# Kernel tuning notes

Measured on AMD Instinct MI355X. Metric: run time of the kernel, lower is better.

Reference implementation:

```python
import jax, jax.numpy as jnp
import numpy as np

B, L, D, H = 2, 2048, 1024, 16
DH = D // H  # dim_head = 64
NEG_INF = 1e12


def setup_inputs() -> dict:
    key = jax.random.key(0)
    ks = jax.random.split(key, 12)
    s_in = 1.0 / np.sqrt(D)
    inp = {
        "q": jax.random.normal(ks[0], (B, L, D), jnp.float32),
        "k": jax.random.normal(ks[1], (B, L, D), jnp.float32),
        "v": jax.random.normal(ks[2], (B, L, D), jnp.float32),
        # causal mask, True = position is masked (matches masked_fill_ semantics)
        "mask": jnp.broadcast_to(
            jnp.triu(jnp.ones((L, L), jnp.bool_), k=1)[None, None], (B, 1, L, L)
        ),
        # torch Linear weight is [out, in]; store transposed [in, out] for x @ W
        "Wq": jax.random.normal(ks[3], (D, D), jnp.float32) * s_in,
        "bq": jnp.zeros((D,), jnp.float32),
        "Wk": jax.random.normal(ks[4], (D, D), jnp.float32) * s_in,
        "bk": jnp.zeros((D,), jnp.float32),
        "Wv": jax.random.normal(ks[5], (D, D), jnp.float32) * s_in,
        "bv": jnp.zeros((D,), jnp.float32),
        "Wo": jax.random.normal(ks[6], (D, D), jnp.float32) * s_in,
        "bo": jnp.zeros((D,), jnp.float32),
    }
    return inp


def _split_heads(x):
    # [b, l, h*d] -> [b, h, l, d]
    b, l, _ = x.shape
    return x.reshape(b, l, H, DH).transpose(0, 2, 1, 3)


def reference(q, k, v, mask, Wq, bq, Wk, bk, Wv, bv, Wo, bo):
    Q = _split_heads(q @ Wq + bq)
    K = _split_heads(k @ Wk + bk)
    V = _split_heads(v @ Wv + bv)
    scale = 1.0 / np.sqrt(DH)
    dots = jnp.einsum("bhqd,bhkd->bhqk", Q, K) * scale  # [b, h, L, L]
    dots = jnp.where(mask, -NEG_INF, dots)
    attn = jax.nn.softmax(dots, axis=-1)
    out = jnp.einsum("bhqk,bhkd->bhqd", attn, V)  # [b, h, L, d]
    out = out.transpose(0, 2, 1, 3).reshape(q.shape[0], q.shape[1], D)
    return out @ Wo + bo
```

## Files before the change

### kernel.cpp

```cpp
#include <hip/hip_runtime.h>
#include <stdint.h>

typedef __bf16 bf16;
typedef bf16 bf16x8 __attribute__((ext_vector_type(8)));
typedef bf16 bf16x4 __attribute__((ext_vector_type(4)));
typedef float f32x4 __attribute__((ext_vector_type(4)));

constexpr int B_ = 2, L_ = 2048, D_ = 1024, H_ = 16, DH_ = 64;
constexpr int M_ = B_ * L_;
constexpr float SCALE = 0.125f;

__device__ __forceinline__ void gload_lds16(const void* g, void* l) {
  __builtin_amdgcn_global_load_lds(
      (const __attribute__((address_space(1))) unsigned int*)g,
      (__attribute__((address_space(3))) unsigned int*)l, 16, 0, 0);
}

__global__ void cast_f32_to_bf16(const float* __restrict__ src,
                                 bf16* __restrict__ dst, int n4) {
  int i = blockIdx.x * blockDim.x + threadIdx.x;
  if (i >= n4) return;
  float4 v = reinterpret_cast<const float4*>(src)[i];
  bf16x4 o;
  o[0] = (bf16)v.x; o[1] = (bf16)v.y; o[2] = (bf16)v.z; o[3] = (bf16)v.w;
  reinterpret_cast<bf16x4*>(dst)[i] = o;
}

__global__ void transpose_cast_w(const float* __restrict__ W, bf16* __restrict__ Wt) {
  __shared__ float tile[32][33];
  int tx = threadIdx.x, ty = threadIdx.y;
  int r0 = blockIdx.y * 32, c0 = blockIdx.x * 32;
#pragma unroll
  for (int i = 0; i < 32; i += 8)
    tile[ty + i][tx] = W[(size_t)(r0 + ty + i) * D_ + c0 + tx];
  __syncthreads();
#pragma unroll
  for (int i = 0; i < 32; i += 8)
    Wt[(size_t)(c0 + ty + i) * D_ + r0 + tx] = (bf16)tile[tx][ty + i];
}

constexpr int BM = 128, BN = 64, BK = 32;

template <int MODE>
__global__ __launch_bounds__(256) void gemm_bf16(
    const bf16* __restrict__ A, const bf16* __restrict__ Bt,
    const float* __restrict__ bias, void* __restrict__ outp) {
  __shared__ bf16 As[BM * BK];
  __shared__ bf16 Bs[BN * BK];
  const int tid = threadIdx.x;
  const int wid = tid >> 6, lane = tid & 63;
  const int lr = lane & 15, lg = lane >> 4;
  const int wr = wid >> 1, wc = wid & 1;
  const int m0 = blockIdx.y * BM, n0 = blockIdx.x * BN;

  f32x4 acc[4][2] = {};

  for (int kt = 0; kt < D_; kt += BK) {
    __syncthreads();
#pragma unroll
    for (int i = 0; i < 2; ++i) {
      int c = (i * 4 + wid) * 64 + lane;
      int row = c >> 2, cs = c & 3;
      gload_lds16(A + (size_t)(m0 + row) * D_ + kt + cs * 8,
                  (char*)As + (i * 4 + wid) * 1024);
    }
    {
      int c = wid * 64 + lane;
      int row = c >> 2, cs = c & 3;
      gload_lds16(Bt + (size_t)(n0 + row) * D_ + kt + cs * 8,
                  (char*)Bs + wid * 1024);
    }
    __syncthreads();

    bf16x8 af[4], bfr[2];
#pragma unroll
    for (int i = 0; i < 4; ++i)
      af[i] = *(const bf16x8*)(As + (wr * 64 + i * 16 + lr) * BK + lg * 8);
#pragma unroll
    for (int j = 0; j < 2; ++j)
      bfr[j] = *(const bf16x8*)(Bs + (wc * 32 + j * 16 + lr) * BK + lg * 8);
#pragma unroll
    for (int i = 0; i < 4; ++i)
#pragma unroll
      for (int j = 0; j < 2; ++j)
        acc[i][j] = __builtin_amdgcn_mfma_f32_16x16x32_bf16(af[i], bfr[j], acc[i][j], 0, 0, 0);
  }

#pragma unroll
  for (int i = 0; i < 4; ++i) {
#pragma unroll
    for (int j = 0; j < 2; ++j) {
      const int n = n0 + wc * 32 + j * 16 + lr;
      const float bn = bias[n];
      const int mbase = m0 + wr * 64 + i * 16 + lg * 4;
      if constexpr (MODE == 2) {
        float* out = (float*)outp;
#pragma unroll
        for (int r = 0; r < 4; ++r)
          out[(size_t)(mbase + r) * D_ + n] = acc[i][j][r] + bn;
      } else if constexpr (MODE == 0) {
        bf16* out = (bf16*)outp;
        const int h = n >> 6, dh = n & 63;
#pragma unroll
        for (int r = 0; r < 4; ++r) {
          int m = mbase + r;
          int b = m >> 11, l = m & (L_ - 1);
          out[((size_t)(b * H_ + h) * L_ + l) * DH_ + dh] = (bf16)(acc[i][j][r] + bn);
        }
      } else {
        bf16* out = (bf16*)outp;
        const int h = n >> 6, dh = n & 63;
        int b = mbase >> 11, l = mbase & (L_ - 1);
        bf16x4 pk;
#pragma unroll
        for (int r = 0; r < 4; ++r) pk[r] = (bf16)(acc[i][j][r] + bn);
        *(bf16x4*)(out + ((size_t)(b * H_ + h) * DH_ + dh) * L_ + l) = pk;
      }
    }
  }
}

__global__ __launch_bounds__(256) void attn_fwd(
    const bf16* __restrict__ Q,
    const bf16* __restrict__ K,
    const bf16* __restrict__ Vt,
    bf16* __restrict__ O) {
  __shared__ bf16 Ks[64 * 64];
  __shared__ bf16 Vs[64 * 64];
  __shared__ bf16 Ps[4][16 * 72];
  const int tid = threadIdx.x;
  const int wid = tid >> 6, lane = tid & 63;
  const int lr = lane & 15, lg = lane >> 4;
  const int qt = (gridDim.x - 1) - blockIdx.x;
  const int h = blockIdx.y, b = blockIdx.z;
  const size_t bh = (size_t)b * H_ + h;

  const bf16* qbase = Q + (bh * L_ + (size_t)qt * 64 + wid * 16) * DH_;
  bf16x8 qf[2];
#pragma unroll
  for (int kk = 0; kk < 2; ++kk)
    qf[kk] = *(const bf16x8*)(qbase + lr * DH_ + kk * 32 + lg * 8);

  f32x4 oacc[4] = {};
  float mrun[4], lrun[4];
#pragma unroll
  for (int r = 0; r < 4; ++r) { mrun[r] = -3.0e38f; lrun[r] = 0.f; }
  const int qrow = qt * 64 + wid * 16 + lg * 4;

  for (int kt = 0; kt <= qt; ++kt) {
    __syncthreads();
#pragma unroll
    for (int i = 0; i < 2; ++i) {
      int c = (i * 4 + wid) * 64 + lane;
      int row = c >> 3, cs = c & 7, g = cs ^ (row & 7);
      gload_lds16(K + (bh * L_ + (size_t)kt * 64 + row) * DH_ + g * 8,
                  (char*)Ks + (i * 4 + wid) * 1024);
      gload_lds16(Vt + (bh * DH_ + row) * L_ + (size_t)kt * 64 + g * 8,
                  (char*)Vs + (i * 4 + wid) * 1024);
    }
    __syncthreads();

    f32x4 s[4] = {};
#pragma unroll
    for (int kk = 0; kk < 2; ++kk)
#pragma unroll
      for (int j = 0; j < 4; ++j) {
        int key = j * 16 + lr;
        int ch = kk * 4 + lg;
        bf16x8 bk = *(const bf16x8*)((char*)Ks + key * 128 + ((ch ^ (key & 7)) << 4));
        s[j] = __builtin_amdgcn_mfma_f32_16x16x32_bf16(qf[kk], bk, s[j], 0, 0, 0);
      }

    if (kt == qt) {
#pragma unroll
      for (int j = 0; j < 4; ++j) {
        int key = kt * 64 + j * 16 + lr;
#pragma unroll
        for (int r = 0; r < 4; ++r)
          s[j][r] = (key > qrow + r) ? -3.0e38f : s[j][r] * SCALE;
      }
    } else {
#pragma unroll
      for (int j = 0; j < 4; ++j)
#pragma unroll
        for (int r = 0; r < 4; ++r) s[j][r] *= SCALE;
    }

    float t[4];
#pragma unroll
    for (int r = 0; r < 4; ++r)
      t[r] = fmaxf(fmaxf(s[0][r], s[1][r]), fmaxf(s[2][r], s[3][r]));
#pragma unroll
    for (int d = 1; d < 16; d <<= 1)
#pragma unroll
      for (int r = 0; r < 4; ++r) t[r] = fmaxf(t[r], __shfl_xor(t[r], d));

    float corr[4];
#pragma unroll
    for (int r = 0; r < 4; ++r) {
      float mn = fmaxf(mrun[r], t[r]);
      corr[r] = __expf(mrun[r] - mn);
      mrun[r] = mn;
    }
    float rs[4] = {0.f, 0.f, 0.f, 0.f};
#pragma unroll
    for (int j = 0; j < 4; ++j)
#pragma unroll
      for (int r = 0; r < 4; ++r) {
        float p = __expf(s[j][r] - mrun[r]);
        s[j][r] = p;
        rs[r] += p;
      }
#pragma unroll
    for (int d = 1; d < 16; d <<= 1)
#pragma unroll
      for (int r = 0; r < 4; ++r) rs[r] += __shfl_xor(rs[r], d);
#pragma unroll
    for (int r = 0; r < 4; ++r) lrun[r] = lrun[r] * corr[r] + rs[r];
#pragma unroll
    for (int j = 0; j < 4; ++j)
#pragma unroll
      for (int r = 0; r < 4; ++r) oacc[j][r] *= corr[r];

    bf16* pw = &Ps[wid][0];
#pragma unroll
    for (int j = 0; j < 4; ++j)
#pragma unroll
      for (int r = 0; r < 4; ++r)
        pw[(lg * 4 + r) * 72 + j * 16 + lr] = (bf16)s[j][r];

    bf16x8 ap[2];
#pragma unroll
    for (int st = 0; st < 2; ++st)
      ap[st] = *(const bf16x8*)(pw + lr * 72 + st * 32 + lg * 8);
#pragma unroll
    for (int j = 0; j < 4; ++j)
#pragma unroll
      for (int st = 0; st < 2; ++st) {
        int dh = j * 16 + lr;
        int ch = st * 4 + lg;
        bf16x8 bv = *(const bf16x8*)((char*)Vs + dh * 128 + ((ch ^ (dh & 7)) << 4));
        oacc[j] = __builtin_amdgcn_mfma_f32_16x16x32_bf16(ap[st], bv, oacc[j], 0, 0, 0);
      }
  }

#pragma unroll
  for (int j = 0; j < 4; ++j) {
#pragma unroll
    for (int r = 0; r < 4; ++r) {
      int q = qrow + r;
      int dh = j * 16 + lr;
      O[((size_t)b * L_ + q) * D_ + h * DH_ + dh] = (bf16)(oacc[j][r] / lrun[r]);
    }
  }
}

extern "C" void kernel_launch(void* const* d_in, const int* in_sizes, int n_in,
                              void* d_out, int out_size, void* d_ws, size_t ws_size,
                              hipStream_t stream) {
  const float* q  = (const float*)d_in[0];
  const float* k  = (const float*)d_in[1];
  const float* v  = (const float*)d_in[2];
  const float* Wq = (const float*)d_in[4];
  const float* bq = (const float*)d_in[5];
  const float* Wk = (const float*)d_in[6];
  const float* bk = (const float*)d_in[7];
  const float* Wv = (const float*)d_in[8];
  const float* bv = (const float*)d_in[9];
  const float* Wo = (const float*)d_in[10];
  const float* bo = (const float*)d_in[11];

  char* ws = (char*)d_ws;
  bf16* castbuf = (bf16*)(ws);
  bf16* WqT = (bf16*)(ws + (8ull << 20));
  bf16* WkT = (bf16*)(ws + (10ull << 20));
  bf16* WvT = (bf16*)(ws + (12ull << 20));
  bf16* WoT = (bf16*)(ws + (14ull << 20));
  bf16* Qb  = (bf16*)(ws + (16ull << 20));
  bf16* Kb  = (bf16*)(ws + (24ull << 20));
  bf16* Vtb = (bf16*)(ws + (32ull << 20));

  dim3 tb(32, 8), tg(D_ / 32, D_ / 32);
  transpose_cast_w<<<tg, tb, 0, stream>>>(Wq, WqT);
  transpose_cast_w<<<tg, tb, 0, stream>>>(Wk, WkT);
  transpose_cast_w<<<tg, tb, 0, stream>>>(Wv, WvT);
  transpose_cast_w<<<tg, tb, 0, stream>>>(Wo, WoT);

  const int n4 = (M_ * D_) / 4;
  dim3 cg((n4 + 255) / 256);
  dim3 gg(D_ / BN, M_ / BM);

  cast_f32_to_bf16<<<cg, 256, 0, stream>>>(q, castbuf, n4);
  gemm_bf16<0><<<gg, 256, 0, stream>>>(castbuf, WqT, bq, Qb);
  cast_f32_to_bf16<<<cg, 256, 0, stream>>>(k, castbuf, n4);
  gemm_bf16<0><<<gg, 256, 0, stream>>>(castbuf, WkT, bk, Kb);
  cast_f32_to_bf16<<<cg, 256, 0, stream>>>(v, castbuf, n4);
  gemm_bf16<1><<<gg, 256, 0, stream>>>(castbuf, WvT, bv, Vtb);

  dim3 ag(L_ / 64, H_, B_);
  attn_fwd<<<ag, 256, 0, stream>>>(Qb, Kb, Vtb, castbuf);

  gemm_bf16<2><<<gg, 256, 0, stream>>>(castbuf, WoT, bo, (float*)d_out);
}
```

Measured before the change: 351.9 us.

## Double-buffer GEMM and attention, pair causal tiles, fold scale into Q, batch cast launches

The GEMM now uses BK=64 with swizzled LDS, double-buffered async loads and a grouped block-index swizzle. The attention kernel becomes a 2-wave block that handles a light and a heavy 32-row query tile together to balance causal work. It also double-buffers K/V, switches to exp2 with the log2e*scale folded into the Q projection, and skips the rescale unless the max grows enough. The casts and weight transposes are merged into single launches with separate buffers. This cuts launch overhead and load stalls, but the lazy-rescale threshold and workspace buffer aliasing add correctness risk.

```diff
diff --git a/kernel.cpp b/kernel.cpp
--- a/kernel.cpp
+++ b/kernel.cpp
@@ -8,26 +8,34 @@
 
 constexpr int B_ = 2, L_ = 2048, D_ = 1024, H_ = 16, DH_ = 64;
 constexpr int M_ = B_ * L_;
-constexpr float SCALE = 0.125f;
+constexpr float QSCALE = 0.125f * 1.44269504f;
 
 __device__ __forceinline__ void gload_lds16(const void* g, void* l) {
   __builtin_amdgcn_global_load_lds(
       (const __attribute__((address_space(1))) unsigned int*)g,
       (__attribute__((address_space(3))) unsigned int*)l, 16, 0, 0);
 }
-
-__global__ void cast_f32_to_bf16(const float* __restrict__ src,
-                                 bf16* __restrict__ dst, int n4) {
-  int i = blockIdx.x * blockDim.x + threadIdx.x;
-  if (i >= n4) return;
-  float4 v = reinterpret_cast<const float4*>(src)[i];
+#define MEMBAR() asm volatile("" ::: "memory")
+__device__ __forceinline__ void block_bar() {
+  MEMBAR(); __builtin_amdgcn_s_barrier(); MEMBAR();
+}
+
+__global__ void cast3(const float* __restrict__ q, const float* __restrict__ k,
+                      const float* __restrict__ v, bf16* __restrict__ dst) {
+  const float* src = blockIdx.y == 0 ? q : (blockIdx.y == 1 ? k : v);
+  size_t i = (size_t)blockIdx.x * blockDim.x + threadIdx.x;
+  float4 val = reinterpret_cast<const float4*>(src)[i];
   bf16x4 o;
-  o[0] = (bf16)v.x; o[1] = (bf16)v.y; o[2] = (bf16)v.z; o[3] = (bf16)v.w;
-  reinterpret_cast<bf16x4*>(dst)[i] = o;
-}
-
-__global__ void transpose_cast_w(const float* __restrict__ W, bf16* __restrict__ Wt) {
+  o[0] = (bf16)val.x; o[1] = (bf16)val.y; o[2] = (bf16)val.z; o[3] = (bf16)val.w;
+  reinterpret_cast<bf16x4*>(dst + (size_t)blockIdx.y * M_ * D_)[i] = o;
+}
+
+__global__ void transpose_cast_w(const float* __restrict__ W0, const float* __restrict__ W1,
+                                 const float* __restrict__ W2, const float* __restrict__ W3,
+                                 bf16* __restrict__ WT) {
   __shared__ float tile[32][33];
+  const float* W = blockIdx.z == 0 ? W0 : blockIdx.z == 1 ? W1 : blockIdx.z == 2 ? W2 : W3;
+  bf16* Wt = WT + (size_t)blockIdx.z * D_ * D_;
   int tx = threadIdx.x, ty = threadIdx.y;
   int r0 = blockIdx.y * 32, c0 = blockIdx.x * 32;
 #pragma unroll
@@ -39,51 +47,75 @@
     Wt[(size_t)(c0 + ty + i) * D_ + r0 + tx] = (bf16)tile[tx][ty + i];
 }
 
-constexpr int BM = 128, BN = 64, BK = 32;
+constexpr int BM = 128, BN = 64, BK = 64;
 
 template <int MODE>
 __global__ __launch_bounds__(256) void gemm_bf16(
     const bf16* __restrict__ A, const bf16* __restrict__ Bt,
-    const float* __restrict__ bias, void* __restrict__ outp) {
-  __shared__ bf16 As[BM * BK];
-  __shared__ bf16 Bs[BN * BK];
+    const float* __restrict__ bias, void* __restrict__ outp, float oscale) {
+  __shared__ bf16 As[2][BM * BK];
+  __shared__ bf16 Bs[2][BN * BK];
   const int tid = threadIdx.x;
   const int wid = tid >> 6, lane = tid & 63;
   const int lr = lane & 15, lg = lane >> 4;
   const int wr = wid >> 1, wc = wid & 1;
-  const int m0 = blockIdx.y * BM, n0 = blockIdx.x * BN;
+
+  const int bidf = blockIdx.y * gridDim.x + blockIdx.x;
+  const int cpx = (gridDim.x * gridDim.y) >> 3;
+  const int swz = (bidf & 7) * cpx + (bidf >> 3);
+  const int n0 = (swz % gridDim.x) * BN, m0 = (swz / gridDim.x) * BM;
 
   f32x4 acc[4][2] = {};
 
-  for (int kt = 0; kt < D_; kt += BK) {
-    __syncthreads();
+  auto stage = [&](int bsel, int kt) {
+#pragma unroll
+    for (int i = 0; i < 4; ++i) {
+      int slot = i * 4 + wid;
+      int c = slot * 64 + lane;
+      int row = c >> 3, cs = c & 7, g = cs ^ (row & 7);
+      gload_lds16(A + (size_t)(m0 + row) * D_ + kt + g * 8, (char*)As[bsel] + slot * 1024);
+    }
 #pragma unroll
     for (int i = 0; i < 2; ++i) {
-      int c = (i * 4 + wid) * 64 + lane;
-      int row = c >> 2, cs = c & 3;
-      gload_lds16(A + (size_t)(m0 + row) * D_ + kt + cs * 8,
-                  (char*)As + (i * 4 + wid) * 1024);
-    }
-    {
-      int c = wid * 64 + lane;
-      int row = c >> 2, cs = c & 3;
-      gload_lds16(Bt + (size_t)(n0 + row) * D_ + kt + cs * 8,
-                  (char*)Bs + wid * 1024);
-    }
-    __syncthreads();
-
-    bf16x8 af[4], bfr[2];
-#pragma unroll
-    for (int i = 0; i < 4; ++i)
-      af[i] = *(const bf16x8*)(As + (wr * 64 + i * 16 + lr) * BK + lg * 8);
-#pragma unroll
-    for (int j = 0; j < 2; ++j)
-      bfr[j] = *(const bf16x8*)(Bs + (wc * 32 + j * 16 + lr) * BK + lg * 8);
-#pragma unroll
-    for (int i = 0; i < 4; ++i)
-#pragma unroll
-      for (int j = 0; j < 2; ++j)
-        acc[i][j] = __builtin_amdgcn_mfma_f32_16x16x32_bf16(af[i], bfr[j], acc[i][j], 0, 0, 0);
+      int slot = i * 4 + wid;
+      int c = slot * 64 + lane;
+      int row = c >> 3, cs = c & 7, g = cs ^ (row & 7);
+      gload_lds16(Bt + (size_t)(n0 + row) * D_ + kt + g * 8, (char*)Bs[bsel] + slot * 1024);
+    }
+  };
+
+  stage(0, 0);
+  for (int t = 0; t < D_ / BK; ++t) {
+    const int cur = t & 1;
+    if (t < D_ / BK - 1) {
+      stage(cur ^ 1, (t + 1) * BK);
+      asm volatile("s_waitcnt vmcnt(6)" ::: "memory");
+    } else {
+      asm volatile("s_waitcnt vmcnt(0)" ::: "memory");
+    }
+    block_bar();
+#pragma unroll
+    for (int kk = 0; kk < 2; ++kk) {
+      bf16x8 af[4], bfr[2];
+#pragma unroll
+      for (int i = 0; i < 4; ++i) {
+        int R = wr * 64 + i * 16 + lr;
+        int ch = (kk * 4 + lg) ^ (R & 7);
+        af[i] = *(const bf16x8*)((char*)As[cur] + R * 128 + ch * 16);
+      }
+#pragma unroll
+      for (int j = 0; j < 2; ++j) {
+        int R = wc * 32 + j * 16 + lr;
+        int ch = (kk * 4 + lg) ^ (R & 7);
+        bfr[j] = *(const bf16x8*)((char*)Bs[cur] + R * 128 + ch * 16);
+      }
+#pragma unroll
+      for (int i = 0; i < 4; ++i)
+#pragma unroll
+        for (int j = 0; j < 2; ++j)
+          acc[i][j] = __builtin_amdgcn_mfma_f32_16x16x32_bf16(af[i], bfr[j], acc[i][j], 0, 0, 0);
+    }
+    block_bar();
   }
 
 #pragma unroll
@@ -105,7 +137,7 @@
         for (int r = 0; r < 4; ++r) {
           int m = mbase + r;
           int b = m >> 11, l = m & (L_ - 1);
-          out[((size_t)(b * H_ + h) * L_ + l) * DH_ + dh] = (bf16)(acc[i][j][r] + bn);
+          out[((size_t)(b * H_ + h) * L_ + l) * DH_ + dh] = (bf16)((acc[i][j][r] + bn) * oscale);
         }
       } else {
         bf16* out = (bf16*)outp;
@@ -120,139 +152,168 @@
   }
 }
 
-__global__ __launch_bounds__(256) void attn_fwd(
+__global__ __launch_bounds__(128, 2) void attn_fwd(
     const bf16* __restrict__ Q,
     const bf16* __restrict__ K,
     const bf16* __restrict__ Vt,
     bf16* __restrict__ O) {
-  __shared__ bf16 Ks[64 * 64];
-  __shared__ bf16 Vs[64 * 64];
-  __shared__ bf16 Ps[4][16 * 72];
+  __shared__ bf16 Ks[2][64 * 64];
+  __shared__ bf16 Vs[2][64 * 64];
+  __shared__ bf16 Ps[2][16 * 72];
   const int tid = threadIdx.x;
   const int wid = tid >> 6, lane = tid & 63;
   const int lr = lane & 15, lg = lane >> 4;
-  const int qt = (gridDim.x - 1) - blockIdx.x;
+  const int x = blockIdx.x;
   const int h = blockIdx.y, b = blockIdx.z;
   const size_t bh = (size_t)b * H_ + h;
-
-  const bf16* qbase = Q + (bh * L_ + (size_t)qt * 64 + wid * 16) * DH_;
-  bf16x8 qf[2];
-#pragma unroll
-  for (int kk = 0; kk < 2; ++kk)
-    qf[kk] = *(const bf16x8*)(qbase + lr * DH_ + kk * 32 + lg * 8);
-
-  f32x4 oacc[4] = {};
-  float mrun[4], lrun[4];
-#pragma unroll
-  for (int r = 0; r < 4; ++r) { mrun[r] = -3.0e38f; lrun[r] = 0.f; }
-  const int qrow = qt * 64 + wid * 16 + lg * 4;
-
-  for (int kt = 0; kt <= qt; ++kt) {
-    __syncthreads();
-#pragma unroll
-    for (int i = 0; i < 2; ++i) {
-      int c = (i * 4 + wid) * 64 + lane;
+  const int qtA = x, qtB = 63 - x;
+  const int qr0A = qtA * 32 + wid * 16, qr0B = qtB * 32 + wid * 16;
+  const int ktmaxA = (qtA * 32 + 31) >> 6, ktmaxB = (qtB * 32 + 31) >> 6;
+
+  bf16x8 qfA[2], qfB[2];
+  {
+    const bf16* qa = Q + (bh * L_ + qr0A) * DH_;
+    const bf16* qb = Q + (bh * L_ + qr0B) * DH_;
+#pragma unroll
+    for (int kk = 0; kk < 2; ++kk) {
+      qfA[kk] = *(const bf16x8*)(qa + lr * DH_ + kk * 32 + lg * 8);
+      qfB[kk] = *(const bf16x8*)(qb + lr * DH_ + kk * 32 + lg * 8);
+    }
+  }
+
+  f32x4 oA[4] = {}, oB[4] = {};
+  float mA[4], lA[4], mB[4], lB[4];
+#pragma unroll
+  for (int r = 0; r < 4; ++r) { mA[r] = mB[r] = -3.0e38f; lA[r] = lB[r] = 0.f; }
+
+  auto stage = [&](int bsel, int kt) {
+    const bf16* kb = K + (bh * L_ + (size_t)kt * 64) * DH_;
+    const bf16* vb = Vt + bh * (size_t)DH_ * L_ + (size_t)kt * 64;
+#pragma unroll
+    for (int i = 0; i < 4; ++i) {
+      int slot = i * 2 + wid;
+      int c = slot * 64 + lane;
       int row = c >> 3, cs = c & 7, g = cs ^ (row & 7);
-      gload_lds16(K + (bh * L_ + (size_t)kt * 64 + row) * DH_ + g * 8,
-                  (char*)Ks + (i * 4 + wid) * 1024);
-      gload_lds16(Vt + (bh * DH_ + row) * L_ + (size_t)kt * 64 + g * 8,
-                  (char*)Vs + (i * 4 + wid) * 1024);
-    }
-    __syncthreads();
-
-    f32x4 s[4] = {};
+      gload_lds16(kb + (size_t)row * DH_ + g * 8, (char*)Ks[bsel] + slot * 1024);
+      gload_lds16(vb + (size_t)row * L_ + g * 8, (char*)Vs[bsel] + slot * 1024);
+    }
+  };
+
+  bf16* pw = &Ps[wid][0];
+
+  auto smx_pv = [&](f32x4* s, float* m, float* l, f32x4* o, int cur) {
+    float t[4];
+#pragma unroll
+    for (int r = 0; r < 4; ++r)
+      t[r] = fmaxf(fmaxf(s[0][r], s[1][r]), fmaxf(s[2][r], s[3][r]));
+#pragma unroll
+    for (int d = 1; d < 16; d <<= 1)
+#pragma unroll
+      for (int r = 0; r < 4; ++r) t[r] = fmaxf(t[r], __shfl_xor(t[r], d));
+    bool need = false;
+#pragma unroll
+    for (int r = 0; r < 4; ++r) need |= (t[r] > m[r] + 11.0f);
+    if (__any(need)) {
+#pragma unroll
+      for (int r = 0; r < 4; ++r) {
+        float mn = fmaxf(m[r], t[r]);
+        float c = exp2f(m[r] - mn);
+        m[r] = mn; l[r] *= c;
+#pragma unroll
+        for (int j = 0; j < 4; ++j) o[j][r] *= c;
+      }
+    }
+    float rs[4] = {0.f, 0.f, 0.f, 0.f};
+#pragma unroll
+    for (int j = 0; j < 4; ++j)
+#pragma unroll
+      for (int r = 0; r < 4; ++r) {
+        float p = exp2f(s[j][r] - m[r]);
+        s[j][r] = p;
+        rs[r] += p;
+      }
+#pragma unroll
+    for (int d = 1; d < 16; d <<= 1)
+#pragma unroll
+      for (int r = 0; r < 4; ++r) rs[r] += __shfl_xor(rs[r], d);
+#pragma unroll
+    for (int r = 0; r < 4; ++r) l[r] += rs[r];
+#pragma unroll
+    for (int j = 0; j < 4; ++j)
+#pragma unroll
+      for (int r = 0; r < 4; ++r)
+        pw[(lg * 4 + r) * 72 + j * 16 + lr] = (bf16)s[j][r];
+    bf16x8 ap[2];
+#pragma unroll
+    for (int st = 0; st < 2; ++st)
+      ap[st] = *(const bf16x8*)(pw + lr * 72 + st * 32 + lg * 8);
+#pragma unroll
+    for (int j = 0; j < 4; ++j)
+#pragma unroll
+      for (int st = 0; st < 2; ++st) {
+        int dh = j * 16 + lr;
+        int ch = (st * 4 + lg) ^ (dh & 7);
+        bf16x8 bv = *(const bf16x8*)((char*)Vs[cur] + dh * 128 + ch * 16);
+        o[j] = __builtin_amdgcn_mfma_f32_16x16x32_bf16(ap[st], bv, o[j], 0, 0, 0);
+      }
+  };
+
+  stage(0, 0);
+  for (int kt = 0; kt <= ktmaxB; ++kt) {
+    const int cur = kt & 1;
+    if (kt < ktmaxB) {
+      stage(cur ^ 1, kt + 1);
+      asm volatile("s_waitcnt vmcnt(8)" ::: "memory");
+    } else {
+      asm volatile("s_waitcnt vmcnt(0)" ::: "memory");
+    }
+    block_bar();
+    const bool actA = (kt <= ktmaxA);
+
+    f32x4 sB[4] = {}, sA[4] = {};
 #pragma unroll
     for (int kk = 0; kk < 2; ++kk)
 #pragma unroll
       for (int j = 0; j < 4; ++j) {
         int key = j * 16 + lr;
-        int ch = kk * 4 + lg;
-        bf16x8 bk = *(const bf16x8*)((char*)Ks + key * 128 + ((ch ^ (key & 7)) << 4));
-        s[j] = __builtin_amdgcn_mfma_f32_16x16x32_bf16(qf[kk], bk, s[j], 0, 0, 0);
-      }
-
-    if (kt == qt) {
+        int ch = (kk * 4 + lg) ^ (key & 7);
+        bf16x8 bk = *(const bf16x8*)((char*)Ks[cur] + key * 128 + ch * 16);
+        sB[j] = __builtin_amdgcn_mfma_f32_16x16x32_bf16(qfB[kk], bk, sB[j], 0, 0, 0);
+        if (actA) sA[j] = __builtin_amdgcn_mfma_f32_16x16x32_bf16(qfA[kk], bk, sA[j], 0, 0, 0);
+      }
+
+    if (kt == ktmaxB) {
 #pragma unroll
       for (int j = 0; j < 4; ++j) {
         int key = kt * 64 + j * 16 + lr;
 #pragma unroll
         for (int r = 0; r < 4; ++r)
-          s[j][r] = (key > qrow + r) ? -3.0e38f : s[j][r] * SCALE;
-      }
-    } else {
-#pragma unroll
-      for (int j = 0; j < 4; ++j)
-#pragma unroll
-        for (int r = 0; r < 4; ++r) s[j][r] *= SCALE;
-    }
-
-    float t[4];
-#pragma unroll
-    for (int r = 0; r < 4; ++r)
-      t[r] = fmaxf(fmaxf(s[0][r], s[1][r]), fmaxf(s[2][r], s[3][r]));
-#pragma unroll
-    for (int d = 1; d < 16; d <<= 1)
-#pragma unroll
-      for (int r = 0; r < 4; ++r) t[r] = fmaxf(t[r], __shfl_xor(t[r], d));
-
-    float corr[4];
+          if (key > qr0B + lg * 4 + r) sB[j][r] = -1.0e30f;
+      }
+    }
+    if (actA && kt == ktmaxA) {
+#pragma unroll
+      for (int j = 0; j < 4; ++j) {
+        int key = kt * 64 + j * 16 + lr;
+#pragma unroll
+        for (int r = 0; r < 4; ++r)
+          if (key > qr0A + lg * 4 + r) sA[j][r] = -1.0e30f;
+      }
+    }
+
+    smx_pv(sB, mB, lB, oB, cur);
+    if (actA) smx_pv(sA, mA, lA, oA, cur);
+    block_bar();
+  }
+
+#pragma unroll
+  for (int j = 0; j < 4; ++j)
 #pragma unroll
     for (int r = 0; r < 4; ++r) {
-      float mn = fmaxf(mrun[r], t[r]);
-      corr[r] = __expf(mrun[r] - mn);
-      mrun[r] = mn;
-    }
-    float rs[4] = {0.f, 0.f, 0.f, 0.f};
-#pragma unroll
-    for (int j = 0; j < 4; ++j)
-#pragma unroll
-      for (int r = 0; r < 4; ++r) {
-        float p = __expf(s[j][r] - mrun[r]);
-        s[j][r] = p;
-        rs[r] += p;
-      }
-#pragma unroll
-    for (int d = 1; d < 16; d <<= 1)
-#pragma unroll
-      for (int r = 0; r < 4; ++r) rs[r] += __shfl_xor(rs[r], d);
-#pragma unroll
-    for (int r = 0; r < 4; ++r) lrun[r] = lrun[r] * corr[r] + rs[r];
-#pragma unroll
-    for (int j = 0; j < 4; ++j)
-#pragma unroll
-      for (int r = 0; r < 4; ++r) oacc[j][r] *= corr[r];
-
-    bf16* pw = &Ps[wid][0];
-#pragma unroll
-    for (int j = 0; j < 4; ++j)
-#pragma unroll
-      for (int r = 0; r < 4; ++r)
-        pw[(lg * 4 + r) * 72 + j * 16 + lr] = (bf16)s[j][r];
-
-    bf16x8 ap[2];
-#pragma unroll
-    for (int st = 0; st < 2; ++st)
-      ap[st] = *(const bf16x8*)(pw + lr * 72 + st * 32 + lg * 8);
-#pragma unroll
-    for (int j = 0; j < 4; ++j)
-#pragma unroll
-      for (int st = 0; st < 2; ++st) {
-        int dh = j * 16 + lr;
-        int ch = st * 4 + lg;
-        bf16x8 bv = *(const bf16x8*)((char*)Vs + dh * 128 + ((ch ^ (dh & 7)) << 4));
-        oacc[j] = __builtin_amdgcn_mfma_f32_16x16x32_bf16(ap[st], bv, oacc[j], 0, 0, 0);
-      }
-  }
-
-#pragma unroll
-  for (int j = 0; j < 4; ++j) {
-#pragma unroll
-    for (int r = 0; r < 4; ++r) {
-      int q = qrow + r;
       int dh = j * 16 + lr;
-      O[((size_t)b * L_ + q) * D_ + h * DH_ + dh] = (bf16)(oacc[j][r] / lrun[r]);
-    }
-  }
+      O[((size_t)b * L_ + qr0A + lg * 4 + r) * D_ + h * DH_ + dh] = (bf16)(oA[j][r] / lA[r]);
+      O[((size_t)b * L_ + qr0B + lg * 4 + r) * D_ + h * DH_ + dh] = (bf16)(oB[j][r] / lB[r]);
+    }
 }
 
 extern "C" void kernel_launch(void* const* d_in, const int* in_sizes, int n_in,
@@ -271,34 +332,24 @@
   const float* bo = (const float*)d_in[11];
 
   char* ws = (char*)d_ws;
-  bf16* castbuf = (bf16*)(ws);
-  bf16* WqT = (bf16*)(ws + (8ull << 20));
-  bf16* WkT = (bf16*)(ws + (10ull << 20));
-  bf16* WvT = (bf16*)(ws + (12ull << 20));
-  bf16* WoT = (bf16*)(ws + (14ull << 20));
-  bf16* Qb  = (bf16*)(ws + (16ull << 20));
-  bf16* Kb  = (bf16*)(ws + (24ull << 20));
-  bf16* Vtb = (bf16*)(ws + (32ull << 20));
-
-  dim3 tb(32, 8), tg(D_ / 32, D_ / 32);
-  transpose_cast_w<<<tg, tb, 0, stream>>>(Wq, WqT);
-  transpose_cast_w<<<tg, tb, 0, stream>>>(Wk, WkT);
-  transpose_cast_w<<<tg, tb, 0, stream>>>(Wv, WvT);
-  transpose_cast_w<<<tg, tb, 0, stream>>>(Wo, WoT);
-
-  const int n4 = (M_ * D_) / 4;
-  dim3 cg((n4 + 255) / 256);
+  bf16* castQ = (bf16*)ws;
+  bf16* castK = (bf16*)(ws + (8ull << 20));
+  bf16* castV = (bf16*)(ws + (16ull << 20));
+  bf16* WT    = (bf16*)(ws + (24ull << 20));
+  bf16* Vtb   = (bf16*)(ws + (32ull << 20));
+  bf16* Kb    = (bf16*)(ws + (16ull << 20));
+  bf16* Qb    = (bf16*)(ws + (8ull << 20));
+  bf16* Ob    = (bf16*)ws;
+
+  transpose_cast_w<<<dim3(32, 32, 4), dim3(32, 8), 0, stream>>>(Wq, Wk, Wv, Wo, WT);
+  cast3<<<dim3((M_ * D_ / 4) / 256, 3), 256, 0, stream>>>(q, k, v, castQ);
+
   dim3 gg(D_ / BN, M_ / BM);
-
-  cast_f32_to_bf16<<<cg, 256, 0, stream>>>(q, castbuf, n4);
-  gemm_bf16<0><<<gg, 256, 0, stream>>>(castbuf, WqT, bq, Qb);
-  cast_f32_to_bf16<<<cg, 256, 0, stream>>>(k, castbuf, n4);
-  gemm_bf16<0><<<gg, 256, 0, stream>>>(castbuf, WkT, bk, Kb);
-  cast_f32_to_bf16<<<cg, 256, 0, stream>>>(v, castbuf, n4);
-  gemm_bf16<1><<<gg, 256, 0, stream>>>(castbuf, WvT, bv, Vtb);
-
-  dim3 ag(L_ / 64, H_, B_);
-  attn_fwd<<<ag, 256, 0, stream>>>(Qb, Kb, Vtb, castbuf);
-
-  gemm_bf16<2><<<gg, 256, 0, stream>>>(castbuf, WoT, bo, (float*)d_out);
-}
+  gemm_bf16<1><<<gg, 256, 0, stream>>>(castV, WT + 2ull * D_ * D_, bv, Vtb, 1.0f);
+  gemm_bf16<0><<<gg, 256, 0, stream>>>(castK, WT + 1ull * D_ * D_, bk, Kb, 1.0f);
+  gemm_bf16<0><<<gg, 256, 0, stream>>>(castQ, WT, bq, Qb, QSCALE);
+
+  attn_fwd<<<dim3(32, H_, B_), 128, 0, stream>>>(Qb, Kb, Vtb, Ob);
+
+  gemm_bf16<2><<<gg, 256, 0, stream>>>(Ob, WT + 3ull * D_ * D_, bo, (float*)d_out, 1.0f);
+}
```

Measured after the change: 286.3 us. 1.23x faster.
